# Kernel tuning notes

Measured on AMD Instinct MI355X. Metric: run time of the kernel, lower is better.

The kernel has to match this reference:

```python
import jax, jax.numpy as jnp
import numpy as np

NUM_CLASSES = 19
MIN_SAMPLES = 1000.0
LOSS_WEIGHT = 1.0
TWO_PI = 2.0 * np.pi


def _nearest_upsample(x, H, W):
    # x: [D, h, w] -> [D, H, W]; matches torch F.interpolate(mode='nearest')
    h, w = x.shape[1], x.shape[2]
    ih = jnp.arange(H) * h // H
    iw = jnp.arange(W) * w // W
    return x[:, ih][:, :, iw]


def _smooth_l1(a, b):
    # F.smooth_l1_loss with beta=1.0, mean reduction
    d = jnp.abs(a - b)
    return jnp.mean(jnp.where(d < 1.0, 0.5 * d * d, d - 0.5))


def setup_inputs() -> dict:
    key = jax.random.key(0)
    k1, k2 = jax.random.split(key)
    feature = jax.random.normal(k1, (1, 64, 128, 128), dtype=jnp.float32)
    label = jax.random.randint(k2, (1, 1, 512, 512), 0, NUM_CLASSES)
    return {"feature": feature, "label": label}


def reference(feature, label):
    D = feature.shape[1]
    H, W = label.shape[2], label.shape[3]
    feat = _nearest_upsample(feature[0], H, W).reshape(D, -1)   # [D, P]
    lab = label[0, 0].reshape(-1)                               # [P]
    ks = jnp.arange(-3, 4, dtype=feat.dtype)                    # 7 gaussian bins

    def per_class(c):
        mask = (lab == c).astype(feat.dtype)                    # [P]
        n = jnp.sum(mask)
        n_safe = jnp.maximum(n, 1.0)
        miu = (feat * mask).sum(1) / n_safe                     # [D]
        var = (((feat - miu[:, None]) ** 2) * mask).sum(1) / n_safe + 1e-10
        std = jnp.sqrt(var)
        var_s = var / 25.0
        bins = miu[:, None] + ks[None, :] * std[:, None]        # [D, 7]
        # KDE: sum over class pixels of N(bin; feat_p, var_s), vectorized over bins
        z2 = (bins[:, :, None] - feat[:, None, :]) ** 2 / var_s[:, None, None]  # [D,7,P]
        sample_values = (jnp.exp(-0.5 * z2) * mask[None, None, :]).sum(-1) / jnp.sqrt(TWO_PI * var_s)[:, None]
        # target computed under no_grad in the original: bin - miu = k*std
        target_values = jax.lax.stop_gradient(
            jnp.exp(-0.5 * ks ** 2)[None, :] / jnp.sqrt(TWO_PI * var)[:, None]
        )
        hist = sample_values / jnp.maximum(sample_values.sum(1, keepdims=True), 1e-30)
        targ = target_values / target_values.sum(1, keepdims=True)
        active = (n >= MIN_SAMPLES).astype(feat.dtype)
        return _smooth_l1(hist, targ) * active, active

    losses, actives = jax.lax.map(per_class, jnp.arange(NUM_CLASSES))
    return LOSS_WEIGHT * jnp.sum(losses) / jnp.sum(actives)
```

## Files before the change

kernel.cpp:

```cpp
#include <hip/hip_runtime.h>
#include <hip/hip_bf16.h>

#define SRC    16384
#define DCH    64
#define NCLS   19
#define NPAIR  (NCLS*DCH)

#if defined(__has_builtin)
#if __has_builtin(__builtin_amdgcn_exp2f)
#define EXP2F(x) __builtin_amdgcn_exp2f(x)
#else
#define EXP2F(x) __exp2f(x)
#endif
#else
#define EXP2F(x) __exp2f(x)
#endif

__global__ __launch_bounds__(256) void hl_count_kernel(
    const int* __restrict__ label, unsigned char* __restrict__ cnt,
    float* __restrict__ psum)
{
    if (blockIdx.x == 0 && threadIdx.x == 0) psum[0] = 0.f;
    int s  = blockIdx.x * 256 + threadIdx.x;
    int sy = s >> 7, sx = s & 127;
    const int4* lab4 = (const int4*)label;
    int l[16];
#pragma unroll
    for (int r = 0; r < 4; r++) {
        int4 v = lab4[(4 * sy + r) * 128 + sx];
        l[4 * r + 0] = v.x; l[4 * r + 1] = v.y;
        l[4 * r + 2] = v.z; l[4 * r + 3] = v.w;
    }
#pragma unroll
    for (int c = 0; c < NCLS; c++) {
        int cc = 0;
#pragma unroll
        for (int j = 0; j < 16; j++) cc += (l[j] == c) ? 1 : 0;
        cnt[c * SRC + s] = (unsigned char)cc;
    }
}

__global__ __launch_bounds__(256, 4) void hl_fused_kernel(
    const float* __restrict__ feature, const unsigned char* __restrict__ cnt,
    int* __restrict__ ncls, float* __restrict__ psum)
{
    int w = blockIdx.x;
    int c = w >> 6, d = w & 63;
    int t = threadIdx.x;
    int wid = t >> 6;

    const float4*       fp4 = (const float4*)(feature + d * SRC);
    const unsigned int* cpu = (const unsigned int*)(cnt + c * SRC);

    float f1 = 0.f, f2 = 0.f;
    int   nc = 0;
#pragma unroll 4
    for (int i = 0; i < 16; i++) {
        int g = i * 256 + t;
        float4       x  = fp4[g];
        unsigned int cv = cpu[g];
        float xs[4] = {x.x, x.y, x.z, x.w};
        float cf[4] = {(float)(cv & 255u), (float)((cv >> 8) & 255u),
                       (float)((cv >> 16) & 255u), (float)(cv >> 24)};
#pragma unroll
        for (int e = 0; e < 4; e++) {
            float wx = cf[e] * xs[e];
            f1 += wx;
            f2 = fmaf(wx, xs[e], f2);
        }
        nc += (cv & 255u) + ((cv >> 8) & 255u) + ((cv >> 16) & 255u) + (cv >> 24);
    }
    double s1 = (double)f1, s2 = (double)f2;
#pragma unroll
    for (int o = 32; o > 0; o >>= 1) {
        s1 += __shfl_down(s1, o);
        s2 += __shfl_down(s2, o);
        nc += __shfl_down(nc, o);
    }
    __shared__ double ps1[4], ps2[4];
    __shared__ int    pn[4];
    __shared__ float  sh_mu, sh_istd;
    __shared__ int    sh_act;
    if ((t & 63) == 0) { ps1[wid] = s1; ps2[wid] = s2; pn[wid] = nc; }
    __syncthreads();
    if (t == 0) {
        double a = ps1[0] + ps1[1] + ps1[2] + ps1[3];
        double b = ps2[0] + ps2[1] + ps2[2] + ps2[3];
        int    n = pn[0] + pn[1] + pn[2] + pn[3];
        double nsafe = (n > 0) ? (double)n : 1.0;
        double mu  = a / nsafe;
        double var = (b - 2.0 * mu * a + mu * mu * (double)n) / nsafe + 1e-10;
        sh_mu   = (float)mu;
        sh_istd = (float)(1.0 / sqrt(var));
        sh_act  = (n >= 1000);
        if (d == 0) ncls[c] = n;
    }
    __syncthreads();
    if (!sh_act) return;
    float istd = sh_istd;
    float nm   = -sh_mu * istd;

    const float C1 = -18.033688011112042f;
    float acc[7] = {0.f, 0.f, 0.f, 0.f, 0.f, 0.f, 0.f};

#pragma unroll 2
    for (int i = 0; i < 16; i++) {
        int g = i * 256 + t;
        float4       x  = fp4[g];
        unsigned int cv = cpu[g];
        float xs[4] = {x.x, x.y, x.z, x.w};
        float cf[4] = {(float)(cv & 255u), (float)((cv >> 8) & 255u),
                       (float)((cv >> 16) & 255u), (float)(cv >> 24)};
#pragma unroll
        for (int e = 0; e < 4; e++) {
            float u = fmaf(xs[e], istd, nm);
            float p = C1 * u;
            float q = p * u;
#pragma unroll
            for (int k = 0; k < 7; k++) {
                float km  = (float)(k - 3);
                float arg = fmaf(p, -2.f * km, q + C1 * km * km);
                acc[k] = fmaf(cf[e], EXP2F(arg), acc[k]);
            }
        }
    }

    __shared__ float part[4][7];
#pragma unroll
    for (int j = 0; j < 7; j++) {
        float v = acc[j];
#pragma unroll
        for (int o = 32; o > 0; o >>= 1) v += __shfl_down(v, o);
        if ((t & 63) == 0) part[wid][j] = v;
    }
    __syncthreads();

    if (t == 0) {
        double e[7], z = 0.0;
#pragma unroll
        for (int k = -3; k <= 3; k++) { e[k + 3] = exp(-0.5 * (double)(k * k)); z += e[k + 3]; }

        float hist[7], S = 0.f;
#pragma unroll
        for (int j = 0; j < 7; j++) {
            hist[j] = part[0][j] + part[1][j] + part[2][j] + part[3][j];
            S += hist[j];
        }
        float Ss = fmaxf(S, 1e-30f);
        float ps = 0.f;
#pragma unroll
        for (int j = 0; j < 7; j++) {
            float dd = fabsf(hist[j] / Ss - (float)(e[j] / z));
            ps += (dd < 1.f) ? 0.5f * dd * dd : (dd - 0.5f);
        }
        atomicAdd(psum, ps);
    }
}

__global__ __launch_bounds__(64) void hl_final_kernel(
    const float* __restrict__ psum, const int* __restrict__ ncls,
    float* __restrict__ out)
{
    if (threadIdx.x == 0) {
        int A = 0;
#pragma unroll
        for (int i = 0; i < NCLS; i++) A += (ncls[i] >= 1000) ? 1 : 0;
        out[0] = (A > 0) ? psum[0] / (448.0f * (float)A) : 0.0f;
    }
}

extern "C" void kernel_launch(void* const* d_in, const int* in_sizes, int n_in,
                              void* d_out, int out_size, void* d_ws, size_t ws_size,
                              hipStream_t stream)
{
    const float* feature = (const float*)d_in[0];
    const int*   label   = (const int*)d_in[1];
    float*       out     = (float*)d_out;

    char* ws = (char*)d_ws;
    unsigned char* cnt  = (unsigned char*)(ws);
    int*           ncls = (int*)(ws + 311296);
    float*         psum = (float*)(ws + 311424);

    hl_count_kernel<<<SRC / 256, 256, 0, stream>>>(label, cnt, psum);
    hl_fused_kernel<<<NPAIR, 256, 0, stream>>>(feature, cnt, ncls, psum);
    hl_final_kernel<<<1, 64, 0, stream>>>(psum, ncls, out);
}
```

Measured before the change: 88.30 us.

## Compact per-class source pixel lists to skip pixels absent from class

The dense per-class count array is replaced by a compacted list for each class. The build kernel uses ballot, popcount and an atomic offset to write (count<<16 | source index) only for source pixels that contain at least one label of that class. The fused kernel then loops only over these list entries, with software-prefetched gathers of the feature values, which cuts the exp-heavy KDE work and the moment pass to roughly the fraction of pixels where the class is present. In exchange it adds a memset launch, per-class block barriers in the build kernel, and scalar gathered loads in place of float4 streaming.

```diff
diff --git a/kernel.cpp b/kernel.cpp
--- a/kernel.cpp
+++ b/kernel.cpp
@@ -16,13 +16,15 @@
 #define EXP2F(x) __exp2f(x)
 #endif
 
-__global__ __launch_bounds__(256) void hl_count_kernel(
-    const int* __restrict__ label, unsigned char* __restrict__ cnt,
-    float* __restrict__ psum)
-{
-    if (blockIdx.x == 0 && threadIdx.x == 0) psum[0] = 0.f;
-    int s  = blockIdx.x * 256 + threadIdx.x;
+__global__ __launch_bounds__(256) void hl_build_kernel(
+    const int* __restrict__ label, unsigned int* __restrict__ list,
+    int* __restrict__ lpos)
+{
+    int t    = threadIdx.x;
+    int s    = blockIdx.x * 256 + t;
+    int lane = t & 63, wv = t >> 6;
     int sy = s >> 7, sx = s & 127;
+
     const int4* lab4 = (const int4*)label;
     int l[16];
 #pragma unroll
@@ -31,62 +33,83 @@
         l[4 * r + 0] = v.x; l[4 * r + 1] = v.y;
         l[4 * r + 2] = v.z; l[4 * r + 3] = v.w;
     }
+    int cc[NCLS];
 #pragma unroll
     for (int c = 0; c < NCLS; c++) {
-        int cc = 0;
-#pragma unroll
-        for (int j = 0; j < 16; j++) cc += (l[j] == c) ? 1 : 0;
-        cnt[c * SRC + s] = (unsigned char)cc;
+        int n = 0;
+#pragma unroll
+        for (int j = 0; j < 16; j++) n += (l[j] == c) ? 1 : 0;
+        cc[c] = n;
+    }
+
+    __shared__ int wsum[4];
+    __shared__ int sh_base;
+    unsigned long long mlt = (1ull << lane) - 1ull;
+
+    for (int c = 0; c < NCLS; c++) {
+        bool pred = cc[c] > 0;
+        unsigned long long b = __ballot(pred);
+        int rw = __popcll(b & mlt);
+        if (lane == 0) wsum[wv] = __popcll(b);
+        __syncthreads();
+        int w0 = wsum[0], w1 = wsum[1], w2 = wsum[2], w3 = wsum[3];
+        int wo = (wv > 0 ? w0 : 0) + (wv > 1 ? w1 : 0) + (wv > 2 ? w2 : 0);
+        if (t == 0) sh_base = atomicAdd(&lpos[c], w0 + w1 + w2 + w3);
+        __syncthreads();
+        if (pred)
+            list[c * SRC + sh_base + wo + rw] =
+                ((unsigned)cc[c] << 16) | (unsigned)s;
+        __syncthreads();
     }
 }
 
 __global__ __launch_bounds__(256, 4) void hl_fused_kernel(
-    const float* __restrict__ feature, const unsigned char* __restrict__ cnt,
-    int* __restrict__ ncls, float* __restrict__ psum)
+    const float* __restrict__ feature, const unsigned int* __restrict__ list,
+    const int* __restrict__ lpos, int* __restrict__ ncls,
+    float* __restrict__ psum)
 {
     int w = blockIdx.x;
     int c = w >> 6, d = w & 63;
     int t = threadIdx.x;
     int wid = t >> 6;
 
-    const float4*       fp4 = (const float4*)(feature + d * SRC);
-    const unsigned int* cpu = (const unsigned int*)(cnt + c * SRC);
-
-    float f1 = 0.f, f2 = 0.f;
-    int   nc = 0;
-#pragma unroll 4
-    for (int i = 0; i < 16; i++) {
-        int g = i * 256 + t;
-        float4       x  = fp4[g];
-        unsigned int cv = cpu[g];
-        float xs[4] = {x.x, x.y, x.z, x.w};
-        float cf[4] = {(float)(cv & 255u), (float)((cv >> 8) & 255u),
-                       (float)((cv >> 16) & 255u), (float)(cv >> 24)};
-#pragma unroll
-        for (int e = 0; e < 4; e++) {
-            float wx = cf[e] * xs[e];
+    int L = lpos[c];
+    const unsigned int* lst = list + c * SRC;
+    const float*        fp  = feature + d * SRC;
+
+    float f1 = 0.f, f2 = 0.f, nf = 0.f;
+    {
+        unsigned e0 = (t < L) ? lst[t] : 0u;
+        float    x0 = fp[e0 & 0xFFFFu];
+        for (int i = t; i < L; i += 256) {
+            int in = i + 256;
+            unsigned e1 = (in < L) ? lst[in] : 0u;
+            float    x1 = fp[e1 & 0xFFFFu];
+            float cv = (float)(e0 >> 16);
+            float wx = cv * x0;
             f1 += wx;
-            f2 = fmaf(wx, xs[e], f2);
-        }
-        nc += (cv & 255u) + ((cv >> 8) & 255u) + ((cv >> 16) & 255u) + (cv >> 24);
+            f2 = fmaf(wx, x0, f2);
+            nf += cv;
+            e0 = e1; x0 = x1;
+        }
     }
     double s1 = (double)f1, s2 = (double)f2;
 #pragma unroll
     for (int o = 32; o > 0; o >>= 1) {
         s1 += __shfl_down(s1, o);
         s2 += __shfl_down(s2, o);
-        nc += __shfl_down(nc, o);
+        nf += __shfl_down(nf, o);
     }
     __shared__ double ps1[4], ps2[4];
-    __shared__ int    pn[4];
+    __shared__ float  pnf[4];
     __shared__ float  sh_mu, sh_istd;
     __shared__ int    sh_act;
-    if ((t & 63) == 0) { ps1[wid] = s1; ps2[wid] = s2; pn[wid] = nc; }
+    if ((t & 63) == 0) { ps1[wid] = s1; ps2[wid] = s2; pnf[wid] = nf; }
     __syncthreads();
     if (t == 0) {
         double a = ps1[0] + ps1[1] + ps1[2] + ps1[3];
         double b = ps2[0] + ps2[1] + ps2[2] + ps2[3];
-        int    n = pn[0] + pn[1] + pn[2] + pn[3];
+        int    n = (int)(pnf[0] + pnf[1] + pnf[2] + pnf[3]);
         double nsafe = (n > 0) ? (double)n : 1.0;
         double mu  = a / nsafe;
         double var = (b - 2.0 * mu * a + mu * mu * (double)n) / nsafe + 1e-10;
@@ -102,26 +125,24 @@
 
     const float C1 = -18.033688011112042f;
     float acc[7] = {0.f, 0.f, 0.f, 0.f, 0.f, 0.f, 0.f};
-
-#pragma unroll 2
-    for (int i = 0; i < 16; i++) {
-        int g = i * 256 + t;
-        float4       x  = fp4[g];
-        unsigned int cv = cpu[g];
-        float xs[4] = {x.x, x.y, x.z, x.w};
-        float cf[4] = {(float)(cv & 255u), (float)((cv >> 8) & 255u),
-                       (float)((cv >> 16) & 255u), (float)(cv >> 24)};
-#pragma unroll
-        for (int e = 0; e < 4; e++) {
-            float u = fmaf(xs[e], istd, nm);
-            float p = C1 * u;
-            float q = p * u;
+    {
+        unsigned e0 = (t < L) ? lst[t] : 0u;
+        float    x0 = fp[e0 & 0xFFFFu];
+        for (int i = t; i < L; i += 256) {
+            int in = i + 256;
+            unsigned e1 = (in < L) ? lst[in] : 0u;
+            float    x1 = fp[e1 & 0xFFFFu];
+            float cv = (float)(e0 >> 16);
+            float u  = fmaf(x0, istd, nm);
+            float p  = C1 * u;
+            float q  = p * u;
 #pragma unroll
             for (int k = 0; k < 7; k++) {
                 float km  = (float)(k - 3);
                 float arg = fmaf(p, -2.f * km, q + C1 * km * km);
-                acc[k] = fmaf(cf[e], EXP2F(arg), acc[k]);
+                acc[k] = fmaf(cv, EXP2F(arg), acc[k]);
             }
+            e0 = e1; x0 = x1;
         }
     }
 
@@ -178,11 +199,13 @@
     float*       out     = (float*)d_out;
 
     char* ws = (char*)d_ws;
-    unsigned char* cnt  = (unsigned char*)(ws);
-    int*           ncls = (int*)(ws + 311296);
-    float*         psum = (float*)(ws + 311424);
-
-    hl_count_kernel<<<SRC / 256, 256, 0, stream>>>(label, cnt, psum);
-    hl_fused_kernel<<<NPAIR, 256, 0, stream>>>(feature, cnt, ncls, psum);
+    unsigned int* list = (unsigned int*)(ws);
+    int*          lpos = (int*)(ws + 1245184);
+    int*          ncls = (int*)(ws + 1245184 + 128);
+    float*        psum = (float*)(ws + 1245184 + 256);
+
+    hipMemsetAsync(ws + 1245184, 0, 260, stream);
+    hl_build_kernel<<<SRC / 256, 256, 0, stream>>>(label, list, lpos);
+    hl_fused_kernel<<<NPAIR, 256, 0, stream>>>(feature, list, lpos, ncls, psum);
     hl_final_kernel<<<1, 64, 0, stream>>>(psum, ncls, out);
 }
```

After: 117.5 us. 1.33x slower.
